# Performance work log

Hardware: AMD Instinct MI355X
Metric: run time of the kernel (lower is better)

The kernel has to match this reference:

```python
import jax, jax.numpy as jnp
import numpy as np

N, E, D, H, ED = 10000, 160000, 512, 256, 16
EPS = 1e-5  # BatchNorm1d eps


def _cgconv(x, src, dst, edge_attr, Wf, bf, Ws, bs, gamma, beta, mean, var):
    # PyG CGConv: z = [x_i, x_j, e_ij]; m = sigmoid(lin_f(z)) * softplus(lin_s(z));
    # aggr='add' at target i; batch_norm (eval mode, running stats) then residual.
    z = jnp.concatenate([x[dst], x[src], edge_attr], axis=1)  # [E, 2D+ED]
    m = jax.nn.sigmoid(z @ Wf + bf) * jax.nn.softplus(z @ Ws + bs)  # [E, D]
    aggr = jax.ops.segment_sum(m, dst, num_segments=x.shape[0])  # [N, D]
    bn = (aggr - mean) * jax.lax.rsqrt(var + EPS) * gamma + beta
    return x + bn


def _gcnconv(x, src, dst, W, b):
    # PyG GCNConv with add_self_loops=True, normalize=True:
    n = x.shape[0]
    deg = jax.ops.segment_sum(jnp.ones((src.shape[0],), x.dtype), dst, num_segments=n) + 1.0
    dinv = jax.lax.rsqrt(deg)  # [N]
    h = x @ W  # [N, out]
    out = jax.ops.segment_sum((dinv[src] * dinv[dst])[:, None] * h[src], dst, num_segments=n)
    out = out + (dinv * dinv)[:, None] * h  # self-loop contribution
    return out + b


def _forward(x, edge_attr, goal_feat,
             cg1_Wf, cg1_bf, cg1_Ws, cg1_bs, cg1_gamma, cg1_beta, cg1_mean, cg1_var,
             cg2_Wf, cg2_bf, cg2_Ws, cg2_bs, cg2_gamma, cg2_beta, cg2_mean, cg2_var,
             gcn3_W, gcn3_b, gcn4_W, gcn4_b, d1_W, d1_b, d2_W, d2_b, src, dst):
    # dropout layers are identity in eval mode (self.training=False)
    x = jax.nn.relu(_cgconv(x, src, dst, edge_attr, cg1_Wf, cg1_bf, cg1_Ws, cg1_bs,
                            cg1_gamma, cg1_beta, cg1_mean, cg1_var))
    x = jax.nn.relu(_cgconv(x, src, dst, edge_attr, cg2_Wf, cg2_bf, cg2_Ws, cg2_bs,
                            cg2_gamma, cg2_beta, cg2_mean, cg2_var))
    x = jax.nn.relu(_gcnconv(x, src, dst, gcn3_W, gcn3_b))
    x = jax.nn.relu(_gcnconv(x, src, dst, gcn4_W, gcn4_b))
    g = jnp.broadcast_to(goal_feat, (x.shape[0], goal_feat.shape[1]))  # repeat(num_nodes, 1)
    h = jax.nn.relu(jnp.concatenate([x, g], axis=1) @ d1_W + d1_b)
    return h @ d2_W + d2_b  # [N, 1]


def setup_inputs() -> dict:
    ks = jax.random.split(jax.random.key(0), 12)
    w = lambda k, s: jax.random.normal(k, s, dtype=jnp.float32) * 0.02
    Z = 2 * D + ED
    return {
        "x": jax.random.normal(ks[0], (N, D), jnp.float32),
        "edge_attr": jax.random.normal(ks[1], (E, ED), jnp.float32),
        "goal_feat": jax.random.normal(ks[2], (1, D), jnp.float32),
        "cg1_Wf": w(ks[3], (Z, D)), "cg1_bf": jnp.zeros((D,), jnp.float32),
        "cg1_Ws": w(ks[4], (Z, D)), "cg1_bs": jnp.zeros((D,), jnp.float32),
        "cg1_gamma": jnp.ones((D,), jnp.float32), "cg1_beta": jnp.zeros((D,), jnp.float32),
        "cg1_mean": jnp.zeros((D,), jnp.float32), "cg1_var": jnp.ones((D,), jnp.float32),
        "cg2_Wf": w(ks[5], (Z, D)), "cg2_bf": jnp.zeros((D,), jnp.float32),
        "cg2_Ws": w(ks[6], (Z, D)), "cg2_bs": jnp.zeros((D,), jnp.float32),
        "cg2_gamma": jnp.ones((D,), jnp.float32), "cg2_beta": jnp.zeros((D,), jnp.float32),
        "cg2_mean": jnp.zeros((D,), jnp.float32), "cg2_var": jnp.ones((D,), jnp.float32),
        "gcn3_W": w(ks[7], (D, H)), "gcn3_b": jnp.zeros((H,), jnp.float32),
        "gcn4_W": w(ks[8], (H, H)), "gcn4_b": jnp.zeros((H,), jnp.float32),
        "d1_W": w(ks[9], (H + D, D)), "d1_b": jnp.zeros((D,), jnp.float32),
        "d2_W": w(ks[10], (D, 1)), "d2_b": jnp.zeros((1,), jnp.float32),
        "edge_index": jax.random.randint(ks[11], (2, E), 0, N, dtype=jnp.int32),
        "batch": jnp.zeros((N,), jnp.int32),
    }


def reference(x, edge_attr, goal_feat,
              cg1_Wf, cg1_bf, cg1_Ws, cg1_bs, cg1_gamma, cg1_beta, cg1_mean, cg1_var,
              cg2_Wf, cg2_bf, cg2_Ws, cg2_bs, cg2_gamma, cg2_beta, cg2_mean, cg2_var,
              gcn3_W, gcn3_b, gcn4_W, gcn4_b, d1_W, d1_b, d2_W, d2_b,
              edge_index, batch):
    src, dst = edge_index[0], edge_index[1]
    return _forward(x, edge_attr, goal_feat,
                    cg1_Wf, cg1_bf, cg1_Ws, cg1_bs, cg1_gamma, cg1_beta, cg1_mean, cg1_var,
                    cg2_Wf, cg2_bf, cg2_Ws, cg2_bs, cg2_gamma, cg2_beta, cg2_mean, cg2_var,
                    gcn3_W, gcn3_b, gcn4_W, gcn4_b, d1_W, d1_b, d2_W, d2_b, src, dst)
```

## Files before the change

### kernel.cpp

```cpp
#include <hip/hip_runtime.h>
#include <math.h>

#define N_NODES 10000
#define N_EDGES 160000
#define DIM 512
#define HDIM 256
#define EDIM 16
#define BN_EPS 1e-5f
#define L2E 1.4426950408889634f
#define LN2 0.6931471805599453f

typedef unsigned short ushort_t;
typedef unsigned int uint_t;
typedef __attribute__((ext_vector_type(8))) short bf16x8;
typedef __attribute__((ext_vector_type(4))) float f32x4;
typedef __attribute__((ext_vector_type(2))) _Float16 half2_t;

__device__ __forceinline__ ushort_t f2bf(float x) {
    uint_t u = __float_as_uint(x);
    uint_t r = (u + 0x7FFF + ((u >> 16) & 1)) >> 16;
    return (ushort_t)r;
}
__device__ __forceinline__ float bf2f(ushort_t h) {
    return __uint_as_float(((uint_t)h) << 16);
}
__device__ __forceinline__ float bflo(uint_t u) {
    return __uint_as_float(u << 16);
}
__device__ __forceinline__ float bfhi(uint_t u) {
    return __uint_as_float(u & 0xffff0000u);
}
__device__ __forceinline__ void gld16(const void* g, void* l) {
    __builtin_amdgcn_global_load_lds(
        (const __attribute__((address_space(1))) unsigned int*)g,
        (__attribute__((address_space(3))) unsigned int*)l, 16, 0, 0);
}
__device__ __forceinline__ half2_t u2h(uint_t u) {
    return __builtin_bit_cast(half2_t, u);
}
__device__ __forceinline__ uint_t pk_f16(float a, float b) {
    return __builtin_bit_cast(uint_t, __builtin_amdgcn_cvt_pkrtz(a, b));
}
__device__ __forceinline__ float fexp2(float x) {
#if __has_builtin(__builtin_amdgcn_exp2f)
    return __builtin_amdgcn_exp2f(x);
#else
    return __expf(x * LN2);
#endif
}
__device__ __forceinline__ float flog2(float x) {
#if __has_builtin(__builtin_amdgcn_logf)
    return __builtin_amdgcn_logf(x);
#else
    return __logf(x) * L2E;
#endif
}
__device__ __forceinline__ void swz(int lid, int gx, int gy, int& bx, int& by) {
    int per = gy * 8;
    int grp = lid / per;
    int rem = lid - grp * per;
    int gsz = min(8, gx - grp * 8);
    by = rem / gsz;
    bx = grp * 8 + (rem - by * gsz);
}

__global__ void k_hist(const int* __restrict__ dst, int* __restrict__ cnt) {
    int e = blockIdx.x * blockDim.x + threadIdx.x;
    if (e < N_EDGES) atomicAdd(&cnt[dst[e]], 1);
}

__global__ __launch_bounds__(1024) void k_scan(int* __restrict__ offs, float* __restrict__ dinv) {
    __shared__ int wsum[16];
    __shared__ int carryS;
    int t = threadIdx.x, lane = t & 63, wv = t >> 6;
    if (t == 0) carryS = 0;
    __syncthreads();
    for (int base = 0; base < N_NODES; base += 1024) {
        int idx = base + t;
        int v = (idx < N_NODES) ? offs[idx] : 0;
        if (idx < N_NODES) dinv[idx] = rsqrtf((float)v + 1.0f);
        int s = v;
#pragma unroll
        for (int off = 1; off < 64; off <<= 1) {
            int u = __shfl_up(s, off, 64);
            if (lane >= off) s += u;
        }
        if (lane == 63) wsum[wv] = s;
        __syncthreads();
        int carry = carryS;
        if (wv == 0) {
            int w = (lane < 16) ? wsum[lane] : 0;
#pragma unroll
            for (int off = 1; off < 16; off <<= 1) {
                int u = __shfl_up(w, off, 64);
                if (lane >= off) w += u;
            }
            if (lane < 16) wsum[lane] = w;
        }
        __syncthreads();
        int wbase = (wv == 0) ? 0 : wsum[wv - 1];
        if (idx < N_NODES) offs[idx] = carry + wbase + s - v;
        int total = wsum[15];
        __syncthreads();
        if (t == 0) carryS = carry + total;
        __syncthreads();
    }
    if (t == 0) offs[N_NODES] = carryS;
}

__global__ void k_scatter(const int* __restrict__ srcv, const int* __restrict__ dstv,
                          const float* __restrict__ ea,
                          const int* __restrict__ offs, const float* __restrict__ dinv,
                          int* __restrict__ cursor,
                          int* __restrict__ srcArr, float* __restrict__ dinvArr,
                          uint_t* __restrict__ eaP) {
    int e = blockIdx.x * blockDim.x + threadIdx.x;
    if (e >= N_EDGES) return;
    int d = dstv[e];
    int p = offs[d] + atomicAdd(&cursor[d], 1);
    int s = srcv[e];
    srcArr[p] = s;
    dinvArr[p] = dinv[s];
    const float* er = ea + (size_t)e * EDIM;
    uint_t pk[8];
#pragma unroll
    for (int k2 = 0; k2 < 8; k2++) pk[k2] = pk_f16(er[2 * k2], er[2 * k2 + 1]);
    uint_t* q = eaP + (size_t)p * 8;
    *(uint4*)q = *(uint4*)&pk[0];
    *(uint4*)(q + 4) = *(uint4*)&pk[4];
}

__global__ __launch_bounds__(256) void k_cvtW(
    const float* __restrict__ Wf0, const float* __restrict__ Ws0,
    const float* __restrict__ Wf1, const float* __restrict__ Ws1,
    const float* __restrict__ g3W, const float* __restrict__ g4W,
    const float* __restrict__ d1W,
    ushort_t* __restrict__ W2cg0, ushort_t* __restrict__ W2cg1,
    ushort_t* __restrict__ W2g3, ushort_t* __restrict__ W2g4,
    ushort_t* __restrict__ W2d1)
{
    __shared__ ushort_t tle[64][72];
    int b = blockIdx.x, t = threadIdx.x;
    const float* src; int ldw, kin0, cin0, ldk, cout0, kout0; ushort_t* out; float scale;
    if (b < 512) {
        int layer = b >> 8, tt = b & 255;
        int g = tt >> 6, rem = tt & 63;
        int ct = rem >> 3, kt = rem & 7;
        const float* Wf = layer ? Wf1 : Wf0;
        const float* Ws = layer ? Ws1 : Ws0;
        src = (g & 1) ? Ws : Wf;
        ldw = 512; kin0 = ((g & 2) ? 512 : 0) + kt * 64; cin0 = ct * 64;
        out = layer ? W2cg1 : W2cg0; ldk = 512;
        cout0 = g * 512 + ct * 64; kout0 = kt * 64;
        scale = L2E;
    } else if (b < 544) {
        int tt = b - 512; int ct = tt >> 3, kt = tt & 7;
        src = g3W; ldw = 256; kin0 = kt * 64; cin0 = ct * 64;
        out = W2g3; ldk = 512; cout0 = ct * 64; kout0 = kt * 64; scale = 1.f;
    } else if (b < 560) {
        int tt = b - 544; int ct = tt >> 2, kt = tt & 3;
        src = g4W; ldw = 256; kin0 = kt * 64; cin0 = ct * 64;
        out = W2g4; ldk = 256; cout0 = ct * 64; kout0 = kt * 64; scale = 1.f;
    } else {
        int tt = b - 560; int ct = tt >> 2, kt = tt & 3;
        src = d1W; ldw = 512; kin0 = kt * 64; cin0 = ct * 64;
        out = W2d1; ldk = 256; cout0 = ct * 64; kout0 = kt * 64; scale = 1.f;
    }
    int c = t & 63;
    int k4 = t >> 6;
#pragma unroll
    for (int i = 0; i < 16; i++) {
        int k = k4 * 16 + i;
        tle[k][c] = f2bf(src[(size_t)(kin0 + k) * ldw + cin0 + c] * scale);
    }
    __syncthreads();
    int cl = t >> 2, kq = t & 3;
    ushort_t tmp[16];
#pragma unroll
    for (int j = 0; j < 16; j++) tmp[j] = tle[kq * 16 + j][cl];
    ushort_t* dst = out + (size_t)(cout0 + cl) * ldk + kout0 + kq * 16;
    *(uint4*)dst = *(uint4*)&tmp[0];
    *(uint4*)(dst + 8) = *(uint4*)&tmp[8];
}

#define MP_WEP   32
#define MP_GV    40
#define MP_END   20040

__global__ __launch_bounds__(256) void k_megaprep(
    const float* __restrict__ x, const float* __restrict__ goal,
    const float* __restrict__ Wf0, const float* __restrict__ Ws0,
    const float* __restrict__ Wf1, const float* __restrict__ Ws1,
    const float* __restrict__ d1W, const float* __restrict__ d1b,
    ushort_t* __restrict__ A2, uint_t* __restrict__ WEP, float* __restrict__ cgv)
{
    int b = blockIdx.x, t = threadIdx.x;
    if (b < MP_WEP) {
        int layer = b >> 4, blk = b & 15;
        int idx = blk * 256 + t;
        int c = idx >> 3, k2 = idx & 7;
        const float* Wf = (layer ? Wf1 : Wf0) + 1024 * 512;
        const float* Ws = (layer ? Ws1 : Ws0) + 1024 * 512;
        uint_t* WEPf = WEP + layer * 8192;
        uint_t* WEPs = WEPf + 4096;
        WEPf[c * 8 + k2] = pk_f16(Wf[(2 * k2) * 512 + c] * L2E, Wf[(2 * k2 + 1) * 512 + c] * L2E);
        WEPs[c * 8 + k2] = pk_f16(Ws[(2 * k2) * 512 + c] * L2E, Ws[(2 * k2 + 1) * 512 + c] * L2E);
    } else if (b < MP_GV) {
        __shared__ float red[256];
        int bb = b - MP_WEP;
        int c = bb * 64 + (t & 63);
        int slice = t >> 6;
        float acc = 0.f;
        for (int i = 0; i < 128; i++) {
            int k = slice * 128 + i;
            acc += goal[k] * d1W[(size_t)(256 + k) * 512 + c];
        }
        red[t] = acc;
        __syncthreads();
        if (t < 128) red[t] += red[t + 128];
        __syncthreads();
        if (t < 64) cgv[c] = red[t] + red[t + 64] + d1b[c];
    } else {
        int idx = (b - MP_GV) * 256 + t;
        if (idx < N_NODES * 512) A2[idx] = f2bf(x[idx]);
    }
}

__global__ __launch_bounds__(256) void k_gemm3(
    const ushort_t* __restrict__ A2, int K, int M,
    const ushort_t* __restrict__ W2t,
    float* __restrict__ outF, ushort_t* __restrict__ outQ,
    const float* __restrict__ bias, int mode, int ldc, int gx, int gy)
{
    __shared__ ushort_t As[128 * 64];
    __shared__ ushort_t Bs[128 * 64];
    int tid = threadIdx.x;
    int lane = tid & 63, w = tid >> 6;
    int wm = w & 1, wn = w >> 1;
    int lrow = lane & 15, quad = lane >> 4;
    int bx, by;
    swz(blockIdx.x, gx, gy, bx, by);
    int row0 = bx * 128, col0 = by * 128;

    f32x4 acc[4][4] = {};

    const ushort_t* ArG[4]; ushort_t* ArL[4];
    const ushort_t* BrG[4]; ushort_t* BrL[4];
#pragma unroll
    for (int p = 0; p < 4; p++) {
        int s = tid + 256 * p;
        int r = s >> 3, k8p = s & 7;
        int k8l = k8p ^ (r & 7);
        int gra = row0 + r; if (gra >= M) gra = M - 1;
        ArG[p] = A2 + (size_t)gra * K + k8l * 8;
        ArL[p] = As + s * 8;
        BrG[p] = W2t + (size_t)(col0 + r) * K + k8l * 8;
        BrL[p] = Bs + s * 8;
    }
    const ushort_t* afp[2][4];
    const ushort_t* bfp[2][4];
#pragma unroll
    for (int sl = 0; sl < 2; sl++)
#pragma unroll
        for (int mt = 0; mt < 4; mt++) {
            int r = wm * 64 + mt * 16 + lrow;
            afp[sl][mt] = As + (r * 8 + ((sl * 4 + quad) ^ (r & 7))) * 8;
            int c = wn * 64 + mt * 16 + lrow;
            bfp[sl][mt] = Bs + (c * 8 + ((sl * 4 + quad) ^ (c & 7))) * 8;
        }

    for (int k0 = 0; k0 < K; k0 += 64) {
        __syncthreads();
#pragma unroll
        for (int p = 0; p < 4; p++) {
            gld16(ArG[p] + k0, ArL[p]);
            gld16(BrG[p] + k0, BrL[p]);
        }
        __syncthreads();
#pragma unroll
        for (int sl = 0; sl < 2; sl++) {
            bf16x8 af[4], bff[4];
#pragma unroll
            for (int i = 0; i < 4; i++) {
                af[i]  = *(const bf16x8*)afp[sl][i];
                bff[i] = *(const bf16x8*)bfp[sl][i];
            }
#pragma unroll
            for (int mt = 0; mt < 4; mt++)
#pragma unroll
                for (int nt = 0; nt < 4; nt++)
                    acc[mt][nt] = __builtin_amdgcn_mfma_f32_16x16x32_bf16(
                        af[mt], bff[nt], acc[mt][nt], 0, 0, 0);
        }
    }

#pragma unroll
    for (int mt = 0; mt < 4; mt++) {
#pragma unroll
        for (int nt = 0; nt < 4; nt++) {
            int gcol = col0 + wn * 64 + nt * 16 + lrow;
#pragma unroll
            for (int r = 0; r < 4; r++) {
                int grow = row0 + wm * 64 + mt * 16 + quad * 4 + r;
                if (grow >= M) continue;
                float v = acc[mt][nt][r];
                if (mode == 1) {
                    if (gcol < 1024) {
                        outF[(size_t)grow * 1024 + gcol] = v;
                    } else {
                        int c = gcol - 1024;
                        int grp = c >> 9, cc = c & 511;
                        int pos = (cc >> 1) * 4 + grp * 2 + (cc & 1);
                        outQ[(size_t)grow * 1024 + pos] = f2bf(v);
                    }
                } else if (mode == 2) {
                    outF[(size_t)grow * ldc + gcol] = fmaxf(v + bias[gcol], 0.f);
                } else {
                    outQ[(size_t)grow * ldc + gcol] = f2bf(v);
                }
            }
        }
    }
}

__global__ __launch_bounds__(256) void k_gemm64(
    const ushort_t* __restrict__ A2, int K, int M,
    const ushort_t* __restrict__ W2t,
    float* __restrict__ outF, ushort_t* __restrict__ outQ,
    const float* __restrict__ bias, int mode, int ldc, int gx, int gy)
{
    __shared__ ushort_t As[64 * 64];
    __shared__ ushort_t Bs[128 * 64];
    int tid = threadIdx.x;
    int lane = tid & 63, w = tid >> 6;
    int lrow = lane & 15, quad = lane >> 4;
    int bx, by;
    swz(blockIdx.x, gx, gy, bx, by);
    int row0 = bx * 64, col0 = by * 128;

    f32x4 acc[4][2] = {};

    const ushort_t* ArG[2]; ushort_t* ArL[2];
    const ushort_t* BrG[4]; ushort_t* BrL[4];
#pragma unroll
    for (int p = 0; p < 2; p++) {
        int s = tid + 256 * p;
        int r = s >> 3, k8p = s & 7;
        int k8l = k8p ^ (r & 7);
        int gra = row0 + r; if (gra >= M) gra = M - 1;
        ArG[p] = A2 + (size_t)gra * K + k8l * 8;
        ArL[p] = As + s * 8;
    }
#pragma unroll
    for (int p = 0; p < 4; p++) {
        int s = tid + 256 * p;
        int r = s >> 3, k8p = s & 7;
        int k8l = k8p ^ (r & 7);
        BrG[p] = W2t + (size_t)(col0 + r) * K + k8l * 8;
        BrL[p] = Bs + s * 8;
    }
    const ushort_t* afp[2][4];
    const ushort_t* bfp[2][2];
#pragma unroll
    for (int sl = 0; sl < 2; sl++) {
#pragma unroll
        for (int mt = 0; mt < 4; mt++) {
            int r = mt * 16 + lrow;
            afp[sl][mt] = As + (r * 8 + ((sl * 4 + quad) ^ (r & 7))) * 8;
        }
#pragma unroll
        for (int nt = 0; nt < 2; nt++) {
            int c = w * 32 + nt * 16 + lrow;
            bfp[sl][nt] = Bs + (c * 8 + ((sl * 4 + quad) ^ (c & 7))) * 8;
        }
    }

    for (int k0 = 0; k0 < K; k0 += 64) {
        __syncthreads();
        gld16(ArG[0] + k0, ArL[0]);
        gld16(ArG[1] + k0, ArL[1]);
#pragma unroll
        for (int p = 0; p < 4; p++) gld16(BrG[p] + k0, BrL[p]);
        __syncthreads();
#pragma unroll
        for (int sl = 0; sl < 2; sl++) {
            bf16x8 af[4], bff[2];
#pragma unroll
            for (int i = 0; i < 4; i++) af[i] = *(const bf16x8*)afp[sl][i];
#pragma unroll
            for (int i = 0; i < 2; i++) bff[i] = *(const bf16x8*)bfp[sl][i];
#pragma unroll
            for (int mt = 0; mt < 4; mt++)
#pragma unroll
                for (int nt = 0; nt < 2; nt++)
                    acc[mt][nt] = __builtin_amdgcn_mfma_f32_16x16x32_bf16(
                        af[mt], bff[nt], acc[mt][nt], 0, 0, 0);
        }
    }

#pragma unroll
    for (int mt = 0; mt < 4; mt++) {
#pragma unroll
        for (int nt = 0; nt < 2; nt++) {
            int gcol = col0 + w * 32 + nt * 16 + lrow;
#pragma unroll
            for (int r = 0; r < 4; r++) {
                int grow = row0 + mt * 16 + quad * 4 + r;
                if (grow >= M) continue;
                float v = acc[mt][nt][r];
                if (mode == 2) outF[(size_t)grow * ldc + gcol] = fmaxf(v + bias[gcol], 0.f);
                else outQ[(size_t)grow * ldc + gcol] = f2bf(v);
            }
        }
    }
}

__global__ __launch_bounds__(256) void k_cg_aggr(
    const float* __restrict__ xin, const float* __restrict__ P,
    const ushort_t* __restrict__ Qi,
    const uint_t* __restrict__ WEPf, const uint_t* __restrict__ WEPs,
    const float* __restrict__ bfv, const float* __restrict__ bsv,
    const float* __restrict__ gamma, const float* __restrict__ beta,
    const float* __restrict__ mean, const float* __restrict__ var,
    const int* __restrict__ offs, const int* __restrict__ srcArr,
    const uint_t* __restrict__ eaP,
    float* __restrict__ xout, ushort_t* __restrict__ A2out)
{
    int i = blockIdx.x;
    int t = threadIdx.x;
    int c0 = 2 * t;
    uint_t wfp[2][8], wsp[2][8];
    {
        const uint_t* pf8 = WEPf + c0 * 8;
        const uint_t* ps8 = WEPs + c0 * 8;
        *(uint4*)&wfp[0][0] = *(const uint4*)(pf8 + 0);
        *(uint4*)&wfp[0][4] = *(const uint4*)(pf8 + 4);
        *(uint4*)&wfp[1][0] = *(const uint4*)(pf8 + 8);
        *(uint4*)&wfp[1][4] = *(const uint4*)(pf8 + 12);
        *(uint4*)&wsp[0][0] = *(const uint4*)(ps8 + 0);
        *(uint4*)&wsp[0][4] = *(const uint4*)(ps8 + 4);
        *(uint4*)&wsp[1][0] = *(const uint4*)(ps8 + 8);
        *(uint4*)&wsp[1][4] = *(const uint4*)(ps8 + 12);
    }
    float2 pf = *(const float2*)&P[(size_t)i * 1024 + c0];
    float2 ps = *(const float2*)&P[(size_t)i * 1024 + 512 + c0];
    float2 bf2 = *(const float2*)&bfv[c0];
    float2 bs2 = *(const float2*)&bsv[c0];
    pf.x = fmaf(bf2.x, L2E, pf.x); pf.y = fmaf(bf2.y, L2E, pf.y);
    ps.x = fmaf(bs2.x, L2E, ps.x); ps.y = fmaf(bs2.y, L2E, ps.y);
    float acc0 = 0.f, acc1 = 0.f;
    int e0 = offs[i], e1 = offs[i + 1];
    __shared__ uint_t sEaP[32][8];
    __shared__ int sSrc[34];
    const ushort_t* Qbase = Qi + 4 * t;
    for (int base = e0; base < e1; base += 32) {
        int g = min(32, e1 - base);
        __syncthreads();
        if (t < 34) {
            int s = 0;
            if (t < g) s = srcArr[base + t];
            sSrc[t] = s;
        }
        {
            int j = t >> 3, k2 = t & 7;
            if (j < g) sEaP[j][k2] = eaP[(size_t)(base + j) * 8 + k2];
        }
        __syncthreads();
        uint2 q0 = *(const uint2*)(Qbase + ((size_t)sSrc[0] << 10));
        uint2 q1 = *(const uint2*)(Qbase + ((size_t)sSrc[1] << 10));
        for (int j = 0; j < g; j++) {
            uint2 qn = *(const uint2*)(Qbase + ((size_t)sSrc[j + 2] << 10));
            uint4 eA = *(const uint4*)&sEaP[j][0];
            uint4 eB = *(const uint4*)&sEaP[j][4];
            float gf0 = pf.x + bflo(q0.x), gf1 = pf.y + bfhi(q0.x);
            float gs0 = ps.x + bflo(q0.y), gs1 = ps.y + bfhi(q0.y);
            uint_t ek[8] = {eA.x, eA.y, eA.z, eA.w, eB.x, eB.y, eB.z, eB.w};
#pragma unroll
            for (int k = 0; k < 8; k++) {
                half2_t e2 = u2h(ek[k]);
                gf0 = __builtin_amdgcn_fdot2(e2, u2h(wfp[0][k]), gf0, false);
                gf1 = __builtin_amdgcn_fdot2(e2, u2h(wfp[1][k]), gf1, false);
                gs0 = __builtin_amdgcn_fdot2(e2, u2h(wsp[0][k]), gs0, false);
                gs1 = __builtin_amdgcn_fdot2(e2, u2h(wsp[1][k]), gs1, false);
            }
            float sg0 = __builtin_amdgcn_rcpf(1.f + fexp2(-gf0));
            float sg1 = __builtin_amdgcn_rcpf(1.f + fexp2(-gf1));
            float sp0 = fmaxf(gs0, 0.f) + flog2(1.f + fexp2(-fabsf(gs0)));
            float sp1 = fmaxf(gs1, 0.f) + flog2(1.f + fexp2(-fabsf(gs1)));
            acc0 = fmaf(sg0, sp0, acc0);
            acc1 = fmaf(sg1, sp1, acc1);
            q0 = q1; q1 = qn;
        }
    }
    acc0 *= LN2;
    acc1 *= LN2;
    size_t ib = (size_t)i * DIM;
    float2 mn = *(const float2*)&mean[c0];
    float2 vr = *(const float2*)&var[c0];
    float2 gm = *(const float2*)&gamma[c0];
    float2 bt = *(const float2*)&beta[c0];
    float2 xi = *(const float2*)&xin[ib + c0];
    float bn0 = (acc0 - mn.x) * rsqrtf(vr.x + BN_EPS) * gm.x + bt.x;
    float bn1 = (acc1 - mn.y) * rsqrtf(vr.y + BN_EPS) * gm.y + bt.y;
    float o0 = fmaxf(xi.x + bn0, 0.f);
    float o1 = fmaxf(xi.y + bn1, 0.f);
    if (xout) *(float2*)&xout[ib + c0] = make_float2(o0, o1);
    ushort_t h0 = f2bf(o0), h1 = f2bf(o1);
    *(uint_t*)(A2out + (size_t)i * 512 + c0) = (uint_t)h0 | ((uint_t)h1 << 16);
}

__global__ __launch_bounds__(128) void k_gcn_aggr(
    const ushort_t* __restrict__ h, const float* __restrict__ dinv,
    const float* __restrict__ bias,
    const int* __restrict__ offs, const int* __restrict__ srcArr,
    const float* __restrict__ dinvArr, ushort_t* __restrict__ A2out)
{
    int i = blockIdx.x;
    int t = threadIdx.x;
    int c0 = 2 * t;
    float acc0 = 0.f, acc1 = 0.f;
    int e0 = offs[i], e1 = offs[i + 1];
    __shared__ int sS[36];
    __shared__ float sD[36];
    for (int base = e0; base < e1; base += 32) {
        int g = min(32, e1 - base);
        __syncthreads();
        if (t < 36) {
            bool ok = (t < g);
            sS[t] = ok ? srcArr[base + t] : 0;
            sD[t] = ok ? dinvArr[base + t] : 0.f;
        }
        __syncthreads();
        uint_t q0 = *(const uint_t*)(h + (size_t)sS[0] * HDIM + c0);
        uint_t q1 = *(const uint_t*)(h + (size_t)sS[1] * HDIM + c0);
        uint_t q2 = *(const uint_t*)(h + (size_t)sS[2] * HDIM + c0);
        uint_t q3 = *(const uint_t*)(h + (size_t)sS[3] * HDIM + c0);
        for (int j = 0; j < g; j++) {
            uint_t qn = *(const uint_t*)(h + (size_t)sS[j + 4] * HDIM + c0);
            acc0 += sD[j] * bflo(q0);
            acc1 += sD[j] * bfhi(q0);
            q0 = q1; q1 = q2; q2 = q3; q3 = qn;
        }
    }
    float di = dinv[i];
    uint_t qi = *(const uint_t*)(h + (size_t)i * HDIM + c0);
    float2 b2 = *(const float2*)&bias[c0];
    float o0 = fmaxf(di * acc0 + di * di * bflo(qi) + b2.x, 0.f);
    float o1 = fmaxf(di * acc1 + di * di * bfhi(qi) + b2.y, 0.f);
    ushort_t h0 = f2bf(o0), h1 = f2bf(o1);
    *(uint_t*)(A2out + (size_t)i * 256 + c0) = (uint_t)h0 | ((uint_t)h1 << 16);
}

__global__ __launch_bounds__(256) void k_final(const float* __restrict__ hd,
                                               const float* __restrict__ w2,
                                               const float* __restrict__ b2,
                                               float* __restrict__ out) {
    int wave = threadIdx.x >> 6, lane = threadIdx.x & 63;
    int i = blockIdx.x * 4 + wave;
    if (i >= N_NODES) return;
    const float* r = hd + (size_t)i * DIM;
    float acc = 0.f;
#pragma unroll
    for (int q = 0; q < 8; q++) acc += r[lane + 64 * q] * w2[lane + 64 * q];
#pragma unroll
    for (int off = 32; off > 0; off >>= 1) acc += __shfl_down(acc, off, 64);
    if (lane == 0) out[i] = acc + b2[0];
}

extern "C" void kernel_launch(void* const* d_in, const int* in_sizes, int n_in,
                              void* d_out, int out_size, void* d_ws, size_t ws_size,
                              hipStream_t stream) {
    (void)in_sizes; (void)n_in; (void)out_size; (void)ws_size;
    const float* x      = (const float*)d_in[0];
    const float* ea     = (const float*)d_in[1];
    const float* goal   = (const float*)d_in[2];
    const float* cgWf[2] = {(const float*)d_in[3],  (const float*)d_in[11]};
    const float* cgbf[2] = {(const float*)d_in[4],  (const float*)d_in[12]};
    const float* cgWs[2] = {(const float*)d_in[5],  (const float*)d_in[13]};
    const float* cgbs[2] = {(const float*)d_in[6],  (const float*)d_in[14]};
    const float* cggm[2] = {(const float*)d_in[7],  (const float*)d_in[15]};
    const float* cgbt[2] = {(const float*)d_in[8],  (const float*)d_in[16]};
    const float* cgmn[2] = {(const float*)d_in[9],  (const float*)d_in[17]};
    const float* cgvr[2] = {(const float*)d_in[10], (const float*)d_in[18]};
    const float* gcn3_W = (const float*)d_in[19];
    const float* gcn3_b = (const float*)d_in[20];
    const float* gcn4_W = (const float*)d_in[21];
    const float* gcn4_b = (const float*)d_in[22];
    const float* d1_W   = (const float*)d_in[23];
    const float* d1_b   = (const float*)d_in[24];
    const float* d2_W   = (const float*)d_in[25];
    const float* d2_b   = (const float*)d_in[26];
    const int*   eidx   = (const int*)d_in[27];
    const int*   srcv   = eidx;
    const int*   dstv   = eidx + N_EDGES;
    float* outp = (float*)d_out;

    char* w = (char*)d_ws;
    float*    Pbuf  = (float*)w;                      w += (size_t)N_NODES * 1024 * 4;
    ushort_t* Qbuf  = (ushort_t*)w;                   w += (size_t)N_NODES * 1024 * 2;
    float*    xB    = (float*)w;                      w += (size_t)N_NODES * 512 * 4;
    ushort_t* A2    = (ushort_t*)w;                   w += (size_t)N_NODES * 512 * 2;
    ushort_t* A3    = (ushort_t*)w;                   w += (size_t)N_NODES * 256 * 2;
    ushort_t* W2cg0 = (ushort_t*)w;                   w += (size_t)2048 * 512 * 2;
    ushort_t* W2cg1 = (ushort_t*)w;                   w += (size_t)2048 * 512 * 2;
    ushort_t* W2g3  = (ushort_t*)w;                   w += (size_t)256 * 512 * 2;
    ushort_t* W2g4  = (ushort_t*)w;                   w += (size_t)256 * 256 * 2;
    ushort_t* W2d1  = (ushort_t*)w;                   w += (size_t)512 * 256 * 2;
    uint_t*   eaP   = (uint_t*)w;                     w += (size_t)N_EDGES * 8 * 4;
    uint_t*   WEP   = (uint_t*)w;                     w += 16384 * 4;
    float*    cgv   = (float*)w;                      w += 512 * 4;
    int*      srcArr  = (int*)w;                      w += N_EDGES * 4;
    float*    dinvArr = (float*)w;                    w += N_EDGES * 4;
    int*      offs    = (int*)w;                      w += (N_NODES + 1) * 4;
    int*      cursor  = (int*)w;                      w += N_NODES * 4;
    float*    dinv    = (float*)w;                    w += N_NODES * 4;
    uint_t* WEPf[2] = {WEP, WEP + 8192};
    uint_t* WEPs[2] = {WEP + 4096, WEP + 12288};
    ushort_t* h3 = (ushort_t*)Pbuf;
    float*    hd = (float*)Qbuf;

    k_cvtW<<<592, 256, 0, stream>>>(cgWf[0], cgWs[0], cgWf[1], cgWs[1],
                                    gcn3_W, gcn4_W, d1_W,
                                    W2cg0, W2cg1, W2g3, W2g4, W2d1);
    k_megaprep<<<MP_END, 256, 0, stream>>>(x, goal,
        cgWf[0], cgWs[0], cgWf[1], cgWs[1], d1_W, d1_b, A2, WEP, cgv);

    hipMemsetAsync(offs, 0, (N_NODES + 1) * sizeof(int), stream);
    hipMemsetAsync(cursor, 0, N_NODES * sizeof(int), stream);
    k_hist<<<(N_EDGES + 255) / 256, 256, 0, stream>>>(dstv, offs);
    k_scan<<<1, 1024, 0, stream>>>(offs, dinv);
    k_scatter<<<(N_EDGES + 255) / 256, 256, 0, stream>>>(srcv, dstv, ea, offs, dinv,
                                                         cursor, srcArr, dinvArr, eaP);

    k_gemm3<<<79 * 16, 256, 0, stream>>>(A2, 512, N_NODES, W2cg0,
                                         Pbuf, Qbuf, nullptr, 1, 0, 79, 16);
    k_cg_aggr<<<N_NODES, 256, 0, stream>>>(x, Pbuf, Qbuf, WEPf[0], WEPs[0],
                                           cgbf[0], cgbs[0],
                                           cggm[0], cgbt[0], cgmn[0], cgvr[0],
                                           offs, srcArr, eaP, xB, A2);
    k_gemm3<<<79 * 16, 256, 0, stream>>>(A2, 512, N_NODES, W2cg1,
                                         Pbuf, Qbuf, nullptr, 1, 0, 79, 16);
    k_cg_aggr<<<N_NODES, 256, 0, stream>>>(xB, Pbuf, Qbuf, WEPf[1], WEPs[1],
                                           cgbf[1], cgbs[1],
                                           cggm[1], cgbt[1], cgmn[1], cgvr[1],
                                           offs, srcArr, eaP, nullptr, A2);

    k_gemm64<<<157 * 2, 256, 0, stream>>>(A2, 512, N_NODES, W2g3,
                                          nullptr, h3, nullptr, 3, HDIM, 157, 2);
    k_gcn_aggr<<<N_NODES, 128, 0, stream>>>(h3, dinv, gcn3_b, offs, srcArr, dinvArr, A3);

    k_gemm64<<<157 * 2, 256, 0, stream>>>(A3, 256, N_NODES, W2g4,
                                          nullptr, h3, nullptr, 3, HDIM, 157, 2);
    k_gcn_aggr<<<N_NODES, 128, 0, stream>>>(h3, dinv, gcn4_b, offs, srcArr, dinvArr, A3);

    k_gemm64<<<157 * 4, 256, 0, stream>>>(A3, 256, N_NODES, W2d1,
                                          hd, nullptr, cgv, 2, DIM, 157, 4);
    k_final<<<(N_NODES + 3) / 4, 256, 0, stream>>>(hd, d2_W, d2_b, outp);
}
```

Baseline: 556.4 us.

## Compute edge-attribute projection in CGConv aggregation with bf16 MFMA tiles

The per-edge 16-dim edge-attribute projection in k_cg_aggr is moved from per-thread fdot2 loops over f16-packed weights to 16x16x32 bf16 MFMA over batches of 16 edges. The results are staged as bf16 in shared memory and then read in the per-edge sigmoid/softplus loop. Edge attributes and the edge weights switch from f16 to bf16 packing to match. This removes register-resident weights and per-edge dot-product ALU work, at the cost of more shared memory, extra synchronisation, halved edge batches, and bf16 rounding of the projected values.

```diff
diff --git a/kernel.cpp b/kernel.cpp
--- a/kernel.cpp
+++ b/kernel.cpp
@@ -14,7 +14,6 @@
 typedef unsigned int uint_t;
 typedef __attribute__((ext_vector_type(8))) short bf16x8;
 typedef __attribute__((ext_vector_type(4))) float f32x4;
-typedef __attribute__((ext_vector_type(2))) _Float16 half2_t;
 
 __device__ __forceinline__ ushort_t f2bf(float x) {
     uint_t u = __float_as_uint(x);
@@ -30,16 +29,13 @@
 __device__ __forceinline__ float bfhi(uint_t u) {
     return __uint_as_float(u & 0xffff0000u);
 }
+__device__ __forceinline__ uint_t pk_bf(float a, float b) {
+    return (uint_t)f2bf(a) | ((uint_t)f2bf(b) << 16);
+}
 __device__ __forceinline__ void gld16(const void* g, void* l) {
     __builtin_amdgcn_global_load_lds(
         (const __attribute__((address_space(1))) unsigned int*)g,
         (__attribute__((address_space(3))) unsigned int*)l, 16, 0, 0);
-}
-__device__ __forceinline__ half2_t u2h(uint_t u) {
-    return __builtin_bit_cast(half2_t, u);
-}
-__device__ __forceinline__ uint_t pk_f16(float a, float b) {
-    return __builtin_bit_cast(uint_t, __builtin_amdgcn_cvt_pkrtz(a, b));
 }
 __device__ __forceinline__ float fexp2(float x) {
 #if __has_builtin(__builtin_amdgcn_exp2f)
@@ -124,7 +120,7 @@
     const float* er = ea + (size_t)e * EDIM;
     uint_t pk[8];
 #pragma unroll
-    for (int k2 = 0; k2 < 8; k2++) pk[k2] = pk_f16(er[2 * k2], er[2 * k2 + 1]);
+    for (int k2 = 0; k2 < 8; k2++) pk[k2] = pk_bf(er[2 * k2], er[2 * k2 + 1]);
     uint_t* q = eaP + (size_t)p * 8;
     *(uint4*)q = *(uint4*)&pk[0];
     *(uint4*)(q + 4) = *(uint4*)&pk[4];
@@ -203,8 +199,8 @@
         const float* Ws = (layer ? Ws1 : Ws0) + 1024 * 512;
         uint_t* WEPf = WEP + layer * 8192;
         uint_t* WEPs = WEPf + 4096;
-        WEPf[c * 8 + k2] = pk_f16(Wf[(2 * k2) * 512 + c] * L2E, Wf[(2 * k2 + 1) * 512 + c] * L2E);
-        WEPs[c * 8 + k2] = pk_f16(Ws[(2 * k2) * 512 + c] * L2E, Ws[(2 * k2 + 1) * 512 + c] * L2E);
+        WEPf[c * 8 + k2] = pk_bf(Wf[(2 * k2) * 512 + c] * L2E, Wf[(2 * k2 + 1) * 512 + c] * L2E);
+        WEPs[c * 8 + k2] = pk_bf(Ws[(2 * k2) * 512 + c] * L2E, Ws[(2 * k2 + 1) * 512 + c] * L2E);
     } else if (b < MP_GV) {
         __shared__ float red[256];
         int bb = b - MP_WEP;
@@ -428,20 +424,13 @@
 {
     int i = blockIdx.x;
     int t = threadIdx.x;
+    int w = t >> 6, lane = t & 63;
+    int lrow = lane & 15, quad = lane >> 4;
     int c0 = 2 * t;
-    uint_t wfp[2][8], wsp[2][8];
-    {
-        const uint_t* pf8 = WEPf + c0 * 8;
-        const uint_t* ps8 = WEPs + c0 * 8;
-        *(uint4*)&wfp[0][0] = *(const uint4*)(pf8 + 0);
-        *(uint4*)&wfp[0][4] = *(const uint4*)(pf8 + 4);
-        *(uint4*)&wfp[1][0] = *(const uint4*)(pf8 + 8);
-        *(uint4*)&wfp[1][4] = *(const uint4*)(pf8 + 12);
-        *(uint4*)&wsp[0][0] = *(const uint4*)(ps8 + 0);
-        *(uint4*)&wsp[0][4] = *(const uint4*)(ps8 + 4);
-        *(uint4*)&wsp[1][0] = *(const uint4*)(ps8 + 8);
-        *(uint4*)&wsp[1][4] = *(const uint4*)(ps8 + 12);
-    }
+    __shared__ uint_t sEaP[16][8];
+    __shared__ int sSrc[18];
+    __shared__ ushort_t sF[16][516];
+    __shared__ ushort_t sG[16][516];
     float2 pf = *(const float2*)&P[(size_t)i * 1024 + c0];
     float2 ps = *(const float2*)&P[(size_t)i * 1024 + 512 + c0];
     float2 bf2 = *(const float2*)&bfv[c0];
@@ -450,39 +439,53 @@
     ps.x = fmaf(bs2.x, L2E, ps.x); ps.y = fmaf(bs2.y, L2E, ps.y);
     float acc0 = 0.f, acc1 = 0.f;
     int e0 = offs[i], e1 = offs[i + 1];
-    __shared__ uint_t sEaP[32][8];
-    __shared__ int sSrc[34];
     const ushort_t* Qbase = Qi + 4 * t;
-    for (int base = e0; base < e1; base += 32) {
-        int g = min(32, e1 - base);
-        __syncthreads();
-        if (t < 34) {
-            int s = 0;
-            if (t < g) s = srcArr[base + t];
-            sSrc[t] = s;
-        }
+    for (int base = e0; base < e1; base += 16) {
+        int g = min(16, e1 - base);
+        __syncthreads();
+        if (t < 18) sSrc[t] = (t < g) ? srcArr[base + t] : 0;
+        if (t >= 32 && t < 160) {
+            int tt = t - 32;
+            int j = tt >> 3, k2 = tt & 7;
+            sEaP[j][k2] = (j < g) ? eaP[(size_t)(base + j) * 8 + k2] : 0u;
+        }
+        __syncthreads();
+        bf16x8 eb;
         {
-            int j = t >> 3, k2 = t & 7;
-            if (j < g) sEaP[j][k2] = eaP[(size_t)(base + j) * 8 + k2];
-        }
-        __syncthreads();
+            uint4 u = make_uint4(0, 0, 0, 0);
+            if (quad < 2) u = *(const uint4*)&sEaP[lrow][(quad & 1) * 4];
+            eb = __builtin_bit_cast(bf16x8, u);
+        }
+#pragma unroll
+        for (int nt = 0; nt < 8; nt++) {
+            int chA = w * 128 + nt * 16 + lrow;
+            uint4 uf = make_uint4(0, 0, 0, 0), us4 = make_uint4(0, 0, 0, 0);
+            if (quad < 2) {
+                uf  = *(const uint4*)&WEPf[chA * 8 + (quad & 1) * 4];
+                us4 = *(const uint4*)&WEPs[chA * 8 + (quad & 1) * 4];
+            }
+            f32x4 cf = {0.f, 0.f, 0.f, 0.f};
+            f32x4 cs = {0.f, 0.f, 0.f, 0.f};
+            cf = __builtin_amdgcn_mfma_f32_16x16x32_bf16(
+                __builtin_bit_cast(bf16x8, uf), eb, cf, 0, 0, 0);
+            cs = __builtin_amdgcn_mfma_f32_16x16x32_bf16(
+                __builtin_bit_cast(bf16x8, us4), eb, cs, 0, 0, 0);
+            int chW = w * 128 + nt * 16 + quad * 4;
+            uint2 pkf = make_uint2(pk_bf(cf[0], cf[1]), pk_bf(cf[2], cf[3]));
+            uint2 pks = make_uint2(pk_bf(cs[0], cs[1]), pk_bf(cs[2], cs[3]));
+            *(uint2*)&sF[lrow][chW] = pkf;
+            *(uint2*)&sG[lrow][chW] = pks;
+        }
         uint2 q0 = *(const uint2*)(Qbase + ((size_t)sSrc[0] << 10));
         uint2 q1 = *(const uint2*)(Qbase + ((size_t)sSrc[1] << 10));
         for (int j = 0; j < g; j++) {
             uint2 qn = *(const uint2*)(Qbase + ((size_t)sSrc[j + 2] << 10));
-            uint4 eA = *(const uint4*)&sEaP[j][0];
-            uint4 eB = *(const uint4*)&sEaP[j][4];
-            float gf0 = pf.x + bflo(q0.x), gf1 = pf.y + bfhi(q0.x);
-            float gs0 = ps.x + bflo(q0.y), gs1 = ps.y + bfhi(q0.y);
-            uint_t ek[8] = {eA.x, eA.y, eA.z, eA.w, eB.x, eB.y, eB.z, eB.w};
-#pragma unroll
-            for (int k = 0; k < 8; k++) {
-                half2_t e2 = u2h(ek[k]);
-                gf0 = __builtin_amdgcn_fdot2(e2, u2h(wfp[0][k]), gf0, false);
-                gf1 = __builtin_amdgcn_fdot2(e2, u2h(wfp[1][k]), gf1, false);
-                gs0 = __builtin_amdgcn_fdot2(e2, u2h(wsp[0][k]), gs0, false);
-                gs1 = __builtin_amdgcn_fdot2(e2, u2h(wsp[1][k]), gs1, false);
-            }
+            uint_t fp = *(const uint_t*)&sF[j][c0];
+            uint_t sp = *(const uint_t*)&sG[j][c0];
+            float gf0 = pf.x + bflo(q0.x) + bflo(fp);
+            float gf1 = pf.y + bfhi(q0.x) + bfhi(fp);
+            float gs0 = ps.x + bflo(q0.y) + bflo(sp);
+            float gs1 = ps.y + bfhi(q0.y) + bfhi(sp);
             float sg0 = __builtin_amdgcn_rcpf(1.f + fexp2(-gf0));
             float sg1 = __builtin_amdgcn_rcpf(1.f + fexp2(-gf1));
             float sp0 = fmaxf(gs0, 0.f) + flog2(1.f + fexp2(-fabsf(gs0)));
@@ -505,8 +508,7 @@
     float o0 = fmaxf(xi.x + bn0, 0.f);
     float o1 = fmaxf(xi.y + bn1, 0.f);
     if (xout) *(float2*)&xout[ib + c0] = make_float2(o0, o1);
-    ushort_t h0 = f2bf(o0), h1 = f2bf(o1);
-    *(uint_t*)(A2out + (size_t)i * 512 + c0) = (uint_t)h0 | ((uint_t)h1 << 16);
+    *(uint_t*)(A2out + (size_t)i * 512 + c0) = pk_bf(o0, o1);
 }
 
 __global__ __launch_bounds__(128) void k_gcn_aggr(
@@ -547,8 +549,7 @@
     float2 b2 = *(const float2*)&bias[c0];
     float o0 = fmaxf(di * acc0 + di * di * bflo(qi) + b2.x, 0.f);
     float o1 = fmaxf(di * acc1 + di * di * bfhi(qi) + b2.y, 0.f);
-    ushort_t h0 = f2bf(o0), h1 = f2bf(o1);
-    *(uint_t*)(A2out + (size_t)i * 256 + c0) = (uint_t)h0 | ((uint_t)h1 << 16);
+    *(uint_t*)(A2out + (size_t)i * 256 + c0) = pk_bf(o0, o1);
 }
 
 __global__ __launch_bounds__(256) void k_final(const float* __restrict__ hd,
```

Result: slower. 625.9 us (+12.5%).

## Fuse final dense projection into d1 GEMM epilogue and fold memsets into weight conversion

Applied to the files above, without the earlier changes.

The last GEMM's epilogue now applies bias and ReLU, multiplies by the d2 weight vector, reduces per row through shared-memory atomics and atomically adds the partial sums into the output. This removes the fp32 hidden buffer write and readback and the separate k_final launch. The offset and cursor memsets and the output zeroing move into extra blocks of the weight-conversion kernel, saving two memset calls. In exchange, float atomic accumulation makes the output order-nondeterministic, and zeroing the output relies on ordering with the later GEMM.

```diff
diff --git a/kernel.cpp b/kernel.cpp
--- a/kernel.cpp
+++ b/kernel.cpp
@@ -30,16 +30,19 @@
 __device__ __forceinline__ float bfhi(uint_t u) {
     return __uint_as_float(u & 0xffff0000u);
 }
+__device__ __forceinline__ uint_t pk_bf(float a, float b) {
+    return (uint_t)f2bf(a) | ((uint_t)f2bf(b) << 16);
+}
+__device__ __forceinline__ half2_t u2h(uint_t u) {
+    return __builtin_bit_cast(half2_t, u);
+}
+__device__ __forceinline__ uint_t pk_f16(float a, float b) {
+    return __builtin_bit_cast(uint_t, __builtin_amdgcn_cvt_pkrtz(a, b));
+}
 __device__ __forceinline__ void gld16(const void* g, void* l) {
     __builtin_amdgcn_global_load_lds(
         (const __attribute__((address_space(1))) unsigned int*)g,
         (__attribute__((address_space(3))) unsigned int*)l, 16, 0, 0);
-}
-__device__ __forceinline__ half2_t u2h(uint_t u) {
-    return __builtin_bit_cast(half2_t, u);
-}
-__device__ __forceinline__ uint_t pk_f16(float a, float b) {
-    return __builtin_bit_cast(uint_t, __builtin_amdgcn_cvt_pkrtz(a, b));
 }
 __device__ __forceinline__ float fexp2(float x) {
 #if __has_builtin(__builtin_amdgcn_exp2f)
@@ -137,10 +140,18 @@
     const float* __restrict__ d1W,
     ushort_t* __restrict__ W2cg0, ushort_t* __restrict__ W2cg1,
     ushort_t* __restrict__ W2g3, ushort_t* __restrict__ W2g4,
-    ushort_t* __restrict__ W2d1)
+    ushort_t* __restrict__ W2d1,
+    int* __restrict__ offsZ, int* __restrict__ curZ, float* __restrict__ outZ)
 {
     __shared__ ushort_t tle[64][72];
     int b = blockIdx.x, t = threadIdx.x;
+    if (b >= 592) {
+        int idx = (b - 592) * 256 + t;
+        if (idx < 10001) offsZ[idx] = 0;
+        else if (idx < 20001) curZ[idx - 10001] = 0;
+        else if (idx < 30001) outZ[idx - 20001] = 0.f;
+        return;
+    }
     const float* src; int ldw, kin0, cin0, ldk, cout0, kout0; ushort_t* out; float scale;
     if (b < 512) {
         int layer = b >> 8, tt = b & 255;
@@ -327,10 +338,13 @@
     const ushort_t* __restrict__ A2, int K, int M,
     const ushort_t* __restrict__ W2t,
     float* __restrict__ outF, ushort_t* __restrict__ outQ,
-    const float* __restrict__ bias, int mode, int ldc, int gx, int gy)
+    const float* __restrict__ bias, int mode, int ldc, int gx, int gy,
+    const float* __restrict__ d2w, const float* __restrict__ d2b,
+    float* __restrict__ outG)
 {
     __shared__ ushort_t As[64 * 64];
     __shared__ ushort_t Bs[128 * 64];
+    __shared__ float part[64];
     int tid = threadIdx.x;
     int lane = tid & 63, w = tid >> 6;
     int lrow = lane & 15, quad = lane >> 4;
@@ -375,6 +389,8 @@
         }
     }
 
+    if (mode == 4 && tid < 64) part[tid] = 0.f;
+
     for (int k0 = 0; k0 < K; k0 += 64) {
         __syncthreads();
         gld16(ArG[0] + k0, ArL[0]);
@@ -396,6 +412,40 @@
                     acc[mt][nt] = __builtin_amdgcn_mfma_f32_16x16x32_bf16(
                         af[mt], bff[nt], acc[mt][nt], 0, 0, 0);
         }
+    }
+
+    if (mode == 4) {
+        float w2c[2], bc[2];
+#pragma unroll
+        for (int nt = 0; nt < 2; nt++) {
+            int gcol = col0 + w * 32 + nt * 16 + lrow;
+            w2c[nt] = d2w[gcol];
+            bc[nt] = bias[gcol];
+        }
+        __syncthreads();
+#pragma unroll
+        for (int mt = 0; mt < 4; mt++) {
+#pragma unroll
+            for (int r = 0; r < 4; r++) {
+                float rp = 0.f;
+#pragma unroll
+                for (int nt = 0; nt < 2; nt++) {
+                    float v = fmaxf(acc[mt][nt][r] + bc[nt], 0.f);
+                    rp = fmaf(v, w2c[nt], rp);
+                }
+                atomicAdd(&part[mt * 16 + quad * 4 + r], rp);
+            }
+        }
+        __syncthreads();
+        if (tid < 64) {
+            int grow = row0 + tid;
+            if (grow < M) {
+                float v = part[tid];
+                if (by == 0) v += d2b[0];
+                atomicAdd(&outG[grow], v);
+            }
+        }
+        return;
     }
 
 #pragma unroll
@@ -505,8 +555,7 @@
     float o0 = fmaxf(xi.x + bn0, 0.f);
     float o1 = fmaxf(xi.y + bn1, 0.f);
     if (xout) *(float2*)&xout[ib + c0] = make_float2(o0, o1);
-    ushort_t h0 = f2bf(o0), h1 = f2bf(o1);
-    *(uint_t*)(A2out + (size_t)i * 512 + c0) = (uint_t)h0 | ((uint_t)h1 << 16);
+    *(uint_t*)(A2out + (size_t)i * 512 + c0) = pk_bf(o0, o1);
 }
 
 __global__ __launch_bounds__(128) void k_gcn_aggr(
@@ -547,24 +596,7 @@
     float2 b2 = *(const float2*)&bias[c0];
     float o0 = fmaxf(di * acc0 + di * di * bflo(qi) + b2.x, 0.f);
     float o1 = fmaxf(di * acc1 + di * di * bfhi(qi) + b2.y, 0.f);
-    ushort_t h0 = f2bf(o0), h1 = f2bf(o1);
-    *(uint_t*)(A2out + (size_t)i * 256 + c0) = (uint_t)h0 | ((uint_t)h1 << 16);
-}
-
-__global__ __launch_bounds__(256) void k_final(const float* __restrict__ hd,
-                                               const float* __restrict__ w2,
-                                               const float* __restrict__ b2,
-                                               float* __restrict__ out) {
-    int wave = threadIdx.x >> 6, lane = threadIdx.x & 63;
-    int i = blockIdx.x * 4 + wave;
-    if (i >= N_NODES) return;
-    const float* r = hd + (size_t)i * DIM;
-    float acc = 0.f;
-#pragma unroll
-    for (int q = 0; q < 8; q++) acc += r[lane + 64 * q] * w2[lane + 64 * q];
-#pragma unroll
-    for (int off = 32; off > 0; off >>= 1) acc += __shfl_down(acc, off, 64);
-    if (lane == 0) out[i] = acc + b2[0];
+    *(uint_t*)(A2out + (size_t)i * 256 + c0) = pk_bf(o0, o1);
 }
 
 extern "C" void kernel_launch(void* const* d_in, const int* in_sizes, int n_in,
@@ -617,16 +649,14 @@
     uint_t* WEPf[2] = {WEP, WEP + 8192};
     uint_t* WEPs[2] = {WEP + 4096, WEP + 12288};
     ushort_t* h3 = (ushort_t*)Pbuf;
-    float*    hd = (float*)Qbuf;
-
-    k_cvtW<<<592, 256, 0, stream>>>(cgWf[0], cgWs[0], cgWf[1], cgWs[1],
+
+    k_cvtW<<<710, 256, 0, stream>>>(cgWf[0], cgWs[0], cgWf[1], cgWs[1],
                                     gcn3_W, gcn4_W, d1_W,
-                                    W2cg0, W2cg1, W2g3, W2g4, W2d1);
+                                    W2cg0, W2cg1, W2g3, W2g4, W2d1,
+                                    offs, cursor, outp);
     k_megaprep<<<MP_END, 256, 0, stream>>>(x, goal,
         cgWf[0], cgWs[0], cgWf[1], cgWs[1], d1_W, d1_b, A2, WEP, cgv);
 
-    hipMemsetAsync(offs, 0, (N_NODES + 1) * sizeof(int), stream);
-    hipMemsetAsync(cursor, 0, N_NODES * sizeof(int), stream);
     k_hist<<<(N_EDGES + 255) / 256, 256, 0, stream>>>(dstv, offs);
     k_scan<<<1, 1024, 0, stream>>>(offs, dinv);
     k_scatter<<<(N_EDGES + 255) / 256, 256, 0, stream>>>(srcv, dstv, ea, offs, dinv,
@@ -646,14 +676,16 @@
                                            offs, srcArr, eaP, nullptr, A2);
 
     k_gemm64<<<157 * 2, 256, 0, stream>>>(A2, 512, N_NODES, W2g3,
-                                          nullptr, h3, nullptr, 3, HDIM, 157, 2);
+                                          nullptr, h3, nullptr, 3, HDIM, 157, 2,
+                                          nullptr, nullptr, nullptr);
     k_gcn_aggr<<<N_NODES, 128, 0, stream>>>(h3, dinv, gcn3_b, offs, srcArr, dinvArr, A3);
 
     k_gemm64<<<157 * 2, 256, 0, stream>>>(A3, 256, N_NODES, W2g4,
-                                          nullptr, h3, nullptr, 3, HDIM, 157, 2);
+                                          nullptr, h3, nullptr, 3, HDIM, 157, 2,
+                                          nullptr, nullptr, nullptr);
     k_gcn_aggr<<<N_NODES, 128, 0, stream>>>(h3, dinv, gcn4_b, offs, srcArr, dinvArr, A3);
 
     k_gemm64<<<157 * 4, 256, 0, stream>>>(A3, 256, N_NODES, W2d1,
-                                          hd, nullptr, cgv, 2, DIM, 157, 4);
-    k_final<<<(N_NODES + 3) / 4, 256, 0, stream>>>(hd, d2_W, d2_b, outp);
-}
+                                          nullptr, nullptr, cgv, 4, DIM, 157, 4,
+                                          d2_W, d2_b, outp);
+}
```

New measurement: 563.1 us. No clear change (+1.2%).
